# Performance work log

Measured on AMD Instinct MI355X. Metric: run time of the kernel, lower is better.

The kernel has to match this reference:

```python
import jax, jax.numpy as jnp
import numpy as np

B, N, D, H = 128, 128, 1024, 8
HD = D // H  # 128; NOTE: N must equal HD due to the module's einsum pattern
SCALE = HD ** -0.5


def _split_heads(x):
    # [b, n, h*d] -> [b, h, n, d]
    b, n, _ = x.shape
    return x.reshape(b, n, H, HD).transpose(0, 2, 1, 3)


def setup_inputs() -> dict:
    key = jax.random.key(0)
    ks = jax.random.split(key, 12)
    s = D ** -0.5
    return {
        "words": jax.random.normal(ks[0], (B, N, D), jnp.float32),
        "position": jax.random.normal(ks[1], (B, N, D), jnp.float32),
        "conscious": jax.random.normal(ks[2], (B, N, D), jnp.float32),
        "Wq_w": jax.random.normal(ks[3], (D, D), jnp.float32) * s,
        "Wk_w": jax.random.normal(ks[4], (D, D), jnp.float32) * s,
        "Wv_w": jax.random.normal(ks[5], (D, D), jnp.float32) * s,
        "Wq_p": jax.random.normal(ks[6], (D, D), jnp.float32) * s,
        "Wk_p": jax.random.normal(ks[7], (D, D), jnp.float32) * s,
        "Wq_c": jax.random.normal(ks[8], (D, D), jnp.float32) * s,
        "Wk_c": jax.random.normal(ks[9], (D, D), jnp.float32) * s,
        "Wo": jax.random.normal(ks[10], (D, D), jnp.float32) * s,
        "bo": jax.random.normal(ks[11], (D,), jnp.float32) * 0.01,
    }


def reference(words, position, conscious, Wq_w, Wk_w, Wv_w, Wq_p, Wk_p, Wq_c, Wk_c, Wo, bo):
    q_w = _split_heads(words @ Wq_w)
    k_w = _split_heads(words @ Wk_w)
    v_w = _split_heads(words @ Wv_w)
    q_p = _split_heads(position @ Wq_p)
    k_p = _split_heads(position @ Wk_p)
    q_c = _split_heads(conscious @ Wq_c)
    k_c = _split_heads(conscious @ Wk_c)

    # Faithful to source: 'b h i j, b h j d -> b h i d' contracts q's head dim
    # with k's seq dim (requires N == HD). Three score streams summed.
    sim = (jnp.einsum('bhij,bhjd->bhid', q_w, k_w)
           + jnp.einsum('bhij,bhjd->bhid', q_p, k_p)
           + jnp.einsum('bhij,bhjd->bhid', q_c, k_c)) * SCALE
    attn = jax.nn.softmax(sim, axis=-1)
    out = jnp.einsum('bhij,bhjd->bhid', attn, v_w)  # [b,h,n,d]
    out = out.transpose(0, 2, 1, 3).reshape(B, N, D)  # merge heads
    return out @ Wo + bo
```

## Files before the change

kernel.cpp:

```cpp
#include <hip/hip_runtime.h>


typedef unsigned short u16;
typedef __attribute__((ext_vector_type(8))) short bf16x8;
typedef __attribute__((ext_vector_type(4))) short bf16x4;
typedef __attribute__((ext_vector_type(4))) float f32x4;

__device__ __forceinline__ float bf2f(u16 x) {
  union { unsigned u; float f; } v;
  v.u = ((unsigned)x) << 16;
  return v.f;
}

__device__ __forceinline__ u16 f2bf(float f) {
  union { float f; unsigned u; } v;
  v.f = f;
  unsigned r = v.u + 0x7fffu + ((v.u >> 16) & 1u);
  return (u16)(r >> 16);
}

__device__ __forceinline__ float ldv(const void* p, size_t i, int f32) {
  return f32 ? ((const float*)p)[i] : bf2f(((const u16*)p)[i]);
}

__device__ __forceinline__ f32x4 MFMA(bf16x8 a, bf16x8 b, f32x4 c) {
  return __builtin_amdgcn_mfma_f32_16x16x32_bf16(a, b, c, 0, 0, 0);
}

#define GLDS16(gp, lp)                                               \
  __builtin_amdgcn_global_load_lds(                                  \
      (const __attribute__((address_space(1))) unsigned int*)(gp),   \
      (__attribute__((address_space(3))) unsigned int*)(lp), 16, 0, 0)

__global__ void detect_dtype(const void* words, int* flag) {
  __shared__ int cnt;
  if (threadIdx.x == 0) cnt = 0;
  __syncthreads();
  const u16* w = (const u16*)words;
  int local = 0;
  for (int i = threadIdx.x; i < 2048; i += 256) {
    const u16 v = w[2 * i];
    const int e = (v >> 7) & 0xFF;
    if (v == 0 || (e >= 0x60 && e <= 0x8F)) local++;
  }
  atomicAdd(&cnt, local);
  __syncthreads();
  if (threadIdx.x == 0) *flag = (cnt >= 1434) ? 0 : 1;
}

__global__ __launch_bounds__(256) void cast_w(
    const void* w0, const void* w1, const void* w2, const void* w3,
    const void* w4, const void* w5, const void* w6, const void* w7,
    u16* __restrict__ WT, const int* __restrict__ flag) {
  __shared__ float t[32][33];
  const int f32 = *flag;
  const int p = blockIdx.z;
  const void* W;
  switch (p) {
    case 0: W = w0; break; case 1: W = w1; break; case 2: W = w2; break;
    case 3: W = w3; break; case 4: W = w4; break; case 5: W = w5; break;
    case 6: W = w6; break; default: W = w7; break;
  }
  const int k0 = blockIdx.y * 32, n0 = blockIdx.x * 32;
  const int tx = threadIdx.x & 31, ry = threadIdx.x >> 5;
  for (int r = ry; r < 32; r += 8)
    t[r][tx] = ldv(W, (size_t)(k0 + r) * 1024 + n0 + tx, f32);
  __syncthreads();
  u16* dst = WT + (size_t)p * 1048576ull;
  for (int r = ry; r < 32; r += 8)
    dst[(size_t)(n0 + r) * 1024 + k0 + tx] = f2bf(t[tx][r]);
}

__global__ __launch_bounds__(256) void cast_a(
    const void* x0, const void* x1, const void* x2, u16* __restrict__ Abf,
    int b0, int chb, const int* __restrict__ flag) {
  const int f32 = *flag;
  const int t = blockIdx.z;
  const void* src = (t == 0) ? x0 : ((t == 1) ? x1 : x2);
  u16* dst = Abf + (size_t)t * (size_t)chb * 131072ull;
  const size_t n4 = (size_t)chb * 32768ull;
  const size_t off = (size_t)b0 * 131072ull;
  const size_t stride = (size_t)gridDim.x * 256ull;
  if (f32) {
    const float4* s = (const float4*)src + off / 4;
    for (size_t i = (size_t)blockIdx.x * 256 + threadIdx.x; i < n4; i += stride) {
      const float4 v = s[i];
      bf16x4 o = { (short)f2bf(v.x), (short)f2bf(v.y),
                   (short)f2bf(v.z), (short)f2bf(v.w) };
      *(bf16x4*)&dst[i * 4] = o;
    }
  } else {
    const bf16x4* s = (const bf16x4*)((const u16*)src + off);
    for (size_t i = (size_t)blockIdx.x * 256 + threadIdx.x; i < n4; i += stride)
      ((bf16x4*)dst)[i] = s[i];
  }
}

__global__ __launch_bounds__(256) void proj_mfma(
    const u16* __restrict__ Abf, const u16* __restrict__ WT,
    u16* __restrict__ P, int chb) {
  __shared__ u16 lsA[128 * 32];
  __shared__ u16 lsB[128 * 32];
  const int p = blockIdx.z;
  const int asel = (p < 3) ? 0 : ((p < 5) ? 1 : 2);
  const u16* A = Abf + (size_t)asel * (size_t)chb * 131072ull;
  const u16* W = WT + (size_t)p * 1048576ull;
  u16* C = P + (size_t)p * (size_t)chb * 131072ull;
  const int tr = (p == 1) | (p == 2) | (p == 4) | (p == 6);
  const int tn = blockIdx.x * 128;
  const int tm = blockIdx.y * 128;
  const int w = threadIdx.x >> 6, l = threadIdx.x & 63;
  const int wm = w >> 1, wn = w & 1;
  const int srow = w * 32 + (l >> 2);
  const int skl = (l & 3) * 8;

  f32x4 acc[4][4] = {};
  for (int kt = 0; kt < 1024; kt += 32) {
    #pragma unroll
    for (int c = 0; c < 2; ++c) {
      GLDS16(&A[(size_t)(tm + srow + c * 16) * 1024 + kt + skl],
             &lsA[(w * 32 + c * 16) * 32]);
      GLDS16(&W[(size_t)(tn + srow + c * 16) * 1024 + kt + skl],
             &lsB[(w * 32 + c * 16) * 32]);
    }
    __syncthreads();
    bf16x8 af[4], bfr[4];
    #pragma unroll
    for (int m = 0; m < 4; ++m)
      af[m] = *(const bf16x8*)&lsA[(wm * 64 + m * 16 + (l & 15)) * 32 + (l >> 4) * 8];
    #pragma unroll
    for (int n = 0; n < 4; ++n)
      bfr[n] = *(const bf16x8*)&lsB[(wn * 64 + n * 16 + (l & 15)) * 32 + (l >> 4) * 8];
    #pragma unroll
    for (int m = 0; m < 4; ++m)
      #pragma unroll
      for (int n = 0; n < 4; ++n)
        acc[m][n] = MFMA(af[m], bfr[n], acc[m][n]);
    __syncthreads();
  }

  if (!tr) {
    #pragma unroll
    for (int m = 0; m < 4; ++m)
      #pragma unroll
      for (int n = 0; n < 4; ++n)
        #pragma unroll
        for (int r = 0; r < 4; ++r) {
          const int row = tm + wm * 64 + m * 16 + (l >> 4) * 4 + r;
          const int col = tn + wn * 64 + n * 16 + (l & 15);
          C[(size_t)row * 1024 + col] = f2bf(acc[m][n][r]);
        }
  } else {
    const size_t tb = ((size_t)blockIdx.y * 8 + blockIdx.x) * 16384ull;
    #pragma unroll
    for (int m = 0; m < 4; ++m)
      #pragma unroll
      for (int n = 0; n < 4; ++n) {
        const int d = wn * 64 + n * 16 + (l & 15);
        const int j0 = wm * 64 + m * 16 + (l >> 4) * 4;
        bf16x4 v = { (short)f2bf(acc[m][n][0]), (short)f2bf(acc[m][n][1]),
                     (short)f2bf(acc[m][n][2]), (short)f2bf(acc[m][n][3]) };
        *(bf16x4*)&C[tb + (size_t)d * 128 + j0] = v;
      }
  }
}

__global__ __launch_bounds__(256) void attn_mfma(
    const u16* __restrict__ P, int chb, u16* __restrict__ merged) {
  __shared__ u16 pl[16384];
  const int h = blockIdx.x, b = blockIdx.y;
  const int w = threadIdx.x >> 6, l = threadIdx.x & 63;
  const size_t MS = (size_t)chb * 131072ull;
  const u16* const Qs[3] = { P, P + 3 * MS, P + 5 * MS };
  const u16* const Ks[3] = { P + 1 * MS, P + 4 * MS, P + 6 * MS };
  const u16* V = P + 2 * MS;
  const size_t qb = (size_t)b * 131072ull + (size_t)h * 128;
  const size_t kb = ((size_t)b * 8 + h) * 16384ull;

  f32x4 acc[2][8] = {};
  #pragma unroll
  for (int kt = 0; kt < 128; kt += 32) {
    #pragma unroll
    for (int t = 0; t < 3; ++t) {
      bf16x8 a[2];
      #pragma unroll
      for (int m = 0; m < 2; ++m)
        a[m] = *(const bf16x8*)&Qs[t][qb + (size_t)(w * 32 + m * 16 + (l & 15)) * 1024
                                       + kt + (l >> 4) * 8];
      #pragma unroll
      for (int n = 0; n < 8; ++n) {
        const bf16x8 bb = *(const bf16x8*)&Ks[t][kb + (size_t)(n * 16 + (l & 15)) * 128
                                                 + kt + (l >> 4) * 8];
        acc[0][n] = MFMA(a[0], bb, acc[0][n]);
        acc[1][n] = MFMA(a[1], bb, acc[1][n]);
      }
    }
  }

  const float SC = 0.08838834764831845f;
  #pragma unroll
  for (int m = 0; m < 2; ++m)
    #pragma unroll
    for (int r = 0; r < 4; ++r) {
      float mx = -3.0e38f;
      #pragma unroll
      for (int n = 0; n < 8; ++n) {
        acc[m][n][r] *= SC;
        mx = fmaxf(mx, acc[m][n][r]);
      }
      #pragma unroll
      for (int s = 1; s < 16; s <<= 1) mx = fmaxf(mx, __shfl_xor(mx, s));
      float sm = 0.f;
      #pragma unroll
      for (int n = 0; n < 8; ++n) {
        const float e = __expf(acc[m][n][r] - mx);
        acc[m][n][r] = e;
        sm += e;
      }
      #pragma unroll
      for (int s = 1; s < 16; s <<= 1) sm += __shfl_xor(sm, s);
      const float inv = 1.f / sm;
      #pragma unroll
      for (int n = 0; n < 8; ++n) acc[m][n][r] *= inv;
    }

  #pragma unroll
  for (int m = 0; m < 2; ++m)
    #pragma unroll
    for (int n = 0; n < 8; ++n)
      #pragma unroll
      for (int r = 0; r < 4; ++r) {
        const int row = w * 32 + m * 16 + (l >> 4) * 4 + r;
        const int col = n * 16 + (l & 15);
        const int byte = (row * 256 + col * 2) ^ ((row & 7) << 4);
        *(u16*)((char*)pl + byte) = f2bf(acc[m][n][r]);
      }
  __syncthreads();

  f32x4 o[2][8] = {};
  #pragma unroll
  for (int kt = 0; kt < 128; kt += 32) {
    bf16x8 a[2];
    #pragma unroll
    for (int m = 0; m < 2; ++m) {
      const int row = w * 32 + m * 16 + (l & 15);
      const int byte = (row * 256 + (kt + (l >> 4) * 8) * 2) ^ ((row & 7) << 4);
      a[m] = *(const bf16x8*)((char*)pl + byte);
    }
    #pragma unroll
    for (int n = 0; n < 8; ++n) {
      const bf16x8 bb = *(const bf16x8*)&V[kb + (size_t)(n * 16 + (l & 15)) * 128
                                           + kt + (l >> 4) * 8];
      o[0][n] = MFMA(a[0], bb, o[0][n]);
      o[1][n] = MFMA(a[1], bb, o[1][n]);
    }
  }

  #pragma unroll
  for (int m = 0; m < 2; ++m)
    #pragma unroll
    for (int n = 0; n < 8; ++n)
      #pragma unroll
      for (int r = 0; r < 4; ++r) {
        const int row = w * 32 + m * 16 + (l >> 4) * 4 + r;
        const int col = n * 16 + (l & 15);
        merged[(size_t)(b * 128 + row) * 1024 + h * 128 + col] = f2bf(o[m][n][r]);
      }
}

__global__ __launch_bounds__(256) void final_mfma(
    const u16* __restrict__ A, const u16* __restrict__ W,
    const void* __restrict__ bias, void* __restrict__ out, int b0,
    const int* __restrict__ flag) {
  __shared__ u16 lsA[128 * 32];
  __shared__ u16 lsB[128 * 32];
  const int f32 = *flag;
  const int tn = blockIdx.x * 128;
  const int tm = blockIdx.y * 128;
  const int w = threadIdx.x >> 6, l = threadIdx.x & 63;
  const int wm = w >> 1, wn = w & 1;
  const int srow = w * 32 + (l >> 2);
  const int skl = (l & 3) * 8;

  f32x4 acc[4][4] = {};
  for (int kt = 0; kt < 1024; kt += 32) {
    #pragma unroll
    for (int c = 0; c < 2; ++c) {
      GLDS16(&A[(size_t)(tm + srow + c * 16) * 1024 + kt + skl],
             &lsA[(w * 32 + c * 16) * 32]);
      GLDS16(&W[(size_t)(tn + srow + c * 16) * 1024 + kt + skl],
             &lsB[(w * 32 + c * 16) * 32]);
    }
    __syncthreads();
    bf16x8 af[4], bfr[4];
    #pragma unroll
    for (int m = 0; m < 4; ++m)
      af[m] = *(const bf16x8*)&lsA[(wm * 64 + m * 16 + (l & 15)) * 32 + (l >> 4) * 8];
    #pragma unroll
    for (int n = 0; n < 4; ++n)
      bfr[n] = *(const bf16x8*)&lsB[(wn * 64 + n * 16 + (l & 15)) * 32 + (l >> 4) * 8];
    #pragma unroll
    for (int m = 0; m < 4; ++m)
      #pragma unroll
      for (int n = 0; n < 4; ++n)
        acc[m][n] = MFMA(af[m], bfr[n], acc[m][n]);
    __syncthreads();
  }

  #pragma unroll
  for (int m = 0; m < 4; ++m)
    #pragma unroll
    for (int n = 0; n < 4; ++n)
      #pragma unroll
      for (int r = 0; r < 4; ++r) {
        const int row = tm + wm * 64 + m * 16 + (l >> 4) * 4 + r;
        const int col = tn + wn * 64 + n * 16 + (l & 15);
        const float rv = acc[m][n][r] + ldv(bias, col, f32);
        const size_t g = (size_t)(b0 * 128 + row) * 1024 + col;
        if (f32) ((float*)out)[g] = rv;
        else ((u16*)out)[g] = f2bf(rv);
      }
}

extern "C" void kernel_launch(void* const* d_in, const int* in_sizes, int n_in,
                              void* d_out, int out_size, void* d_ws, size_t ws_size,
                              hipStream_t stream) {
  const size_t fixed = 64ull + 8ull * 1048576ull * 2ull;
  int CHB = 128;
  while (CHB > 1 && fixed + 11ull * (size_t)CHB * 131072ull * 2ull > ws_size)
    CHB >>= 1;

  int* flag = (int*)d_ws;
  u16* WT = (u16*)((char*)d_ws + 64);
  u16* Abf = WT + 8ull * 1048576ull;
  u16* P = Abf + 3ull * (size_t)CHB * 131072ull;
  u16* merged = P + 7ull * (size_t)CHB * 131072ull;

  detect_dtype<<<1, 256, 0, stream>>>(d_in[0], flag);
  cast_w<<<dim3(32, 32, 8), 256, 0, stream>>>(
      d_in[3], d_in[4], d_in[5], d_in[6], d_in[7], d_in[8], d_in[9], d_in[10],
      WT, flag);

  for (int b0 = 0; b0 < 128; b0 += CHB) {
    cast_a<<<dim3(512, 1, 3), 256, 0, stream>>>(
        d_in[0], d_in[1], d_in[2], Abf, b0, CHB, flag);
    proj_mfma<<<dim3(8, CHB, 7), 256, 0, stream>>>(Abf, WT, P, CHB);
    attn_mfma<<<dim3(8, CHB), 256, 0, stream>>>(P, CHB, merged);
    final_mfma<<<dim3(8, CHB), 256, 0, stream>>>(
        merged, WT + 7ull * 1048576ull, d_in[11], d_out, b0, flag);
  }
}
```

Before: 875.6 us.

## Double GEMM K-tile, XOR-swizzle LDS layout, and remap workgroups for L2 locality

Both projection and output GEMMs now stage 64-wide K tiles instead of 32, halving barrier and loop overhead per MFMA. The LDS layout uses an XOR swizzle on 16-byte chunks, applied both to the global source address and to fragment reads, to reduce bank conflicts on the bf16x8 fragment reads. Workgroup IDs are remapped so consecutive blocks walk down M within a column of N, aiming for better L2 reuse of the weight tile. LDS usage doubles per block, which may lower occupancy.

```diff
diff --git a/kernel.cpp b/kernel.cpp
--- a/kernel.cpp
+++ b/kernel.cpp
@@ -31,6 +31,11 @@
   __builtin_amdgcn_global_load_lds(                                  \
       (const __attribute__((address_space(1))) unsigned int*)(gp),   \
       (__attribute__((address_space(3))) unsigned int*)(lp), 16, 0, 0)
+
+__device__ __forceinline__ bf16x8 lds_frag(const u16* ls, int row, int cb) {
+  const int byte = (row * 128 + cb) ^ ((row & 7) << 4);
+  return *(const bf16x8*)((const char*)ls + byte);
+}
 
 __global__ void detect_dtype(const void* words, int* flag) {
   __shared__ int cnt;
@@ -99,43 +104,54 @@
 __global__ __launch_bounds__(256) void proj_mfma(
     const u16* __restrict__ Abf, const u16* __restrict__ WT,
     u16* __restrict__ P, int chb) {
-  __shared__ u16 lsA[128 * 32];
-  __shared__ u16 lsB[128 * 32];
+  __shared__ u16 lsA[128 * 64];
+  __shared__ u16 lsB[128 * 64];
   const int p = blockIdx.z;
   const int asel = (p < 3) ? 0 : ((p < 5) ? 1 : 2);
   const u16* A = Abf + (size_t)asel * (size_t)chb * 131072ull;
   const u16* W = WT + (size_t)p * 1048576ull;
   u16* C = P + (size_t)p * (size_t)chb * 131072ull;
   const int tr = (p == 1) | (p == 2) | (p == 4) | (p == 6);
-  const int tn = blockIdx.x * 128;
-  const int tm = blockIdx.y * 128;
+
+  int wg = blockIdx.y * 8 + blockIdx.x;
+  const int nwg = (int)gridDim.y * 8;
+  wg = (wg & 7) * (nwg >> 3) + (wg >> 3);
+  const int bx = wg & 7, by = wg >> 3;
+
+  const int tn = bx * 128;
+  const int tm = by * 128;
   const int w = threadIdx.x >> 6, l = threadIdx.x & 63;
   const int wm = w >> 1, wn = w & 1;
-  const int srow = w * 32 + (l >> 2);
-  const int skl = (l & 3) * 8;
+  const int lr = l >> 3;
+  const int lc = ((l & 7) * 16) ^ (lr << 4);
+  const int fr = l & 15, fq = l >> 4;
 
   f32x4 acc[4][4] = {};
-  for (int kt = 0; kt < 1024; kt += 32) {
-    #pragma unroll
-    for (int c = 0; c < 2; ++c) {
-      GLDS16(&A[(size_t)(tm + srow + c * 16) * 1024 + kt + skl],
-             &lsA[(w * 32 + c * 16) * 32]);
-      GLDS16(&W[(size_t)(tn + srow + c * 16) * 1024 + kt + skl],
-             &lsB[(w * 32 + c * 16) * 32]);
+  for (int kt = 0; kt < 1024; kt += 64) {
+    #pragma unroll
+    for (int c = 0; c < 4; ++c) {
+      GLDS16(&A[(size_t)(tm + w * 32 + c * 8 + lr) * 1024 + kt + (lc >> 1)],
+             &lsA[(w * 32 + c * 8) * 64]);
+      GLDS16(&W[(size_t)(tn + w * 32 + c * 8 + lr) * 1024 + kt + (lc >> 1)],
+             &lsB[(w * 32 + c * 8) * 64]);
     }
     __syncthreads();
-    bf16x8 af[4], bfr[4];
-    #pragma unroll
-    for (int m = 0; m < 4; ++m)
-      af[m] = *(const bf16x8*)&lsA[(wm * 64 + m * 16 + (l & 15)) * 32 + (l >> 4) * 8];
-    #pragma unroll
-    for (int n = 0; n < 4; ++n)
-      bfr[n] = *(const bf16x8*)&lsB[(wn * 64 + n * 16 + (l & 15)) * 32 + (l >> 4) * 8];
-    #pragma unroll
-    for (int m = 0; m < 4; ++m)
+    #pragma unroll
+    for (int ks = 0; ks < 2; ++ks) {
+      bf16x8 af[4], bfr[4];
+      const int cb = ks * 64 + fq * 16;
+      #pragma unroll
+      for (int m = 0; m < 4; ++m)
+        af[m] = lds_frag(lsA, wm * 64 + m * 16 + fr, cb);
       #pragma unroll
       for (int n = 0; n < 4; ++n)
-        acc[m][n] = MFMA(af[m], bfr[n], acc[m][n]);
+        bfr[n] = lds_frag(lsB, wn * 64 + n * 16 + fr, cb);
+      #pragma unroll
+      for (int m = 0; m < 4; ++m)
+        #pragma unroll
+        for (int n = 0; n < 4; ++n)
+          acc[m][n] = MFMA(af[m], bfr[n], acc[m][n]);
+    }
     __syncthreads();
   }
 
@@ -146,18 +162,18 @@
       for (int n = 0; n < 4; ++n)
         #pragma unroll
         for (int r = 0; r < 4; ++r) {
-          const int row = tm + wm * 64 + m * 16 + (l >> 4) * 4 + r;
-          const int col = tn + wn * 64 + n * 16 + (l & 15);
+          const int row = tm + wm * 64 + m * 16 + fq * 4 + r;
+          const int col = tn + wn * 64 + n * 16 + fr;
           C[(size_t)row * 1024 + col] = f2bf(acc[m][n][r]);
         }
   } else {
-    const size_t tb = ((size_t)blockIdx.y * 8 + blockIdx.x) * 16384ull;
+    const size_t tb = ((size_t)by * 8 + bx) * 16384ull;
     #pragma unroll
     for (int m = 0; m < 4; ++m)
       #pragma unroll
       for (int n = 0; n < 4; ++n) {
-        const int d = wn * 64 + n * 16 + (l & 15);
-        const int j0 = wm * 64 + m * 16 + (l >> 4) * 4;
+        const int d = wn * 64 + n * 16 + fr;
+        const int j0 = wm * 64 + m * 16 + fq * 4;
         bf16x4 v = { (short)f2bf(acc[m][n][0]), (short)f2bf(acc[m][n][1]),
                      (short)f2bf(acc[m][n][2]), (short)f2bf(acc[m][n][3]) };
         *(bf16x4*)&C[tb + (size_t)d * 128 + j0] = v;
@@ -272,49 +288,60 @@
     const u16* __restrict__ A, const u16* __restrict__ W,
     const void* __restrict__ bias, void* __restrict__ out, int b0,
     const int* __restrict__ flag) {
-  __shared__ u16 lsA[128 * 32];
-  __shared__ u16 lsB[128 * 32];
+  __shared__ u16 lsA[128 * 64];
+  __shared__ u16 lsB[128 * 64];
   const int f32 = *flag;
-  const int tn = blockIdx.x * 128;
-  const int tm = blockIdx.y * 128;
+
+  int wg = blockIdx.y * 8 + blockIdx.x;
+  const int nwg = (int)gridDim.y * 8;
+  wg = (wg & 7) * (nwg >> 3) + (wg >> 3);
+  const int bx = wg & 7, by = wg >> 3;
+
+  const int tn = bx * 128;
+  const int tm = by * 128;
   const int w = threadIdx.x >> 6, l = threadIdx.x & 63;
   const int wm = w >> 1, wn = w & 1;
-  const int srow = w * 32 + (l >> 2);
-  const int skl = (l & 3) * 8;
+  const int lr = l >> 3;
+  const int lc = ((l & 7) * 16) ^ (lr << 4);
+  const int fr = l & 15, fq = l >> 4;
 
   f32x4 acc[4][4] = {};
-  for (int kt = 0; kt < 1024; kt += 32) {
-    #pragma unroll
-    for (int c = 0; c < 2; ++c) {
-      GLDS16(&A[(size_t)(tm + srow + c * 16) * 1024 + kt + skl],
-             &lsA[(w * 32 + c * 16) * 32]);
-      GLDS16(&W[(size_t)(tn + srow + c * 16) * 1024 + kt + skl],
-             &lsB[(w * 32 + c * 16) * 32]);
+  for (int kt = 0; kt < 1024; kt += 64) {
+    #pragma unroll
+    for (int c = 0; c < 4; ++c) {
+      GLDS16(&A[(size_t)(tm + w * 32 + c * 8 + lr) * 1024 + kt + (lc >> 1)],
+             &lsA[(w * 32 + c * 8) * 64]);
+      GLDS16(&W[(size_t)(tn + w * 32 + c * 8 + lr) * 1024 + kt + (lc >> 1)],
+             &lsB[(w * 32 + c * 8) * 64]);
     }
     __syncthreads();
-    bf16x8 af[4], bfr[4];
-    #pragma unroll
-    for (int m = 0; m < 4; ++m)
-      af[m] = *(const bf16x8*)&lsA[(wm * 64 + m * 16 + (l & 15)) * 32 + (l >> 4) * 8];
+    #pragma unroll
+    for (int ks = 0; ks < 2; ++ks) {
+      bf16x8 af[4], bfr[4];
+      const int cb = ks * 64 + fq * 16;
+      #pragma unroll
+      for (int m = 0; m < 4; ++m)
+        af[m] = lds_frag(lsA, wm * 64 + m * 16 + fr, cb);
+      #pragma unroll
+      for (int n = 0; n < 4; ++n)
+        bfr[n] = lds_frag(lsB, wn * 64 + n * 16 + fr, cb);
+      #pragma unroll
+      for (int m = 0; m < 4; ++m)
+        #pragma unroll
+        for (int n = 0; n < 4; ++n)
+          acc[m][n] = MFMA(af[m], bfr[n], acc[m][n]);
+    }
+    __syncthreads();
+  }
+
+  #pragma unroll
+  for (int m = 0; m < 4; ++m)
     #pragma unroll
     for (int n = 0; n < 4; ++n)
-      bfr[n] = *(const bf16x8*)&lsB[(wn * 64 + n * 16 + (l & 15)) * 32 + (l >> 4) * 8];
-    #pragma unroll
-    for (int m = 0; m < 4; ++m)
-      #pragma unroll
-      for (int n = 0; n < 4; ++n)
-        acc[m][n] = MFMA(af[m], bfr[n], acc[m][n]);
-    __syncthreads();
-  }
-
-  #pragma unroll
-  for (int m = 0; m < 4; ++m)
-    #pragma unroll
-    for (int n = 0; n < 4; ++n)
       #pragma unroll
       for (int r = 0; r < 4; ++r) {
-        const int row = tm + wm * 64 + m * 16 + (l >> 4) * 4 + r;
-        const int col = tn + wn * 64 + n * 16 + (l & 15);
+        const int row = tm + wm * 64 + m * 16 + fq * 4 + r;
+        const int col = tn + wn * 64 + n * 16 + fr;
         const float rv = acc[m][n][r] + ldv(bias, col, f32);
         const size_t g = (size_t)(b0 * 128 + row) * 1024 + col;
         if (f32) ((float*)out)[g] = rv;
```

After: 834.8 us. 1.05x faster.
